# Kernel optimization log

Measured on AMD Instinct MI355X. Metric: run time of the kernel, lower is better.

The kernel has to match this reference:

```python
import jax, jax.numpy as jnp
import numpy as np


def setup_inputs() -> dict:
    key = jax.random.key(0)
    k1, k2, k3 = jax.random.split(key, 3)
    B, C_in, H, W = 16, 256, 64, 64
    C_out, KH, KW = 256, 3, 3
    x = jax.random.normal(k1, (B, C_in, H, W), dtype=jnp.float32)
    # kaiming-uniform-like scale for realism
    fan_in = C_in * KH * KW
    bound = 1.0 / np.sqrt(fan_in)
    weights = jax.random.normal(k2, (C_out, C_in, KH, KW), dtype=jnp.float32) * bound
    bias = jax.random.uniform(k3, (C_out,), dtype=jnp.float32, minval=-bound, maxval=bound)
    return {"x": x, "weights": weights, "bias": bias}


def reference(x, weights, bias):
    # Conv2dApproximation with approximation_enable=False is an exact conv2d:
    # input is unfolded to [B, C*kh*kw, oh, ow], weights to [C_out, C*kh*kw],
    # and the MultiApp kernel performs the exact MAC (see exact matmul backward).
    # stride=(1,1), padding=(0,0), dilation=(1,1) per init_kwargs.
    out = jax.lax.conv_general_dilated(
        x, weights,
        window_strides=(1, 1),
        padding=((0, 0), (0, 0)),
        rhs_dilation=(1, 1),
        dimension_numbers=("NCHW", "OIHW", "NCHW"),
    )
    return out + bias[None, :, None, None]
```

## Files before the change

kernel.cpp:

```cpp
#include <hip/hip_runtime.h>
#include <stdint.h>

typedef short short8 __attribute__((ext_vector_type(8)));
typedef float f32x4 __attribute__((ext_vector_type(4)));

#define AS1 __attribute__((address_space(1)))
#define AS3 __attribute__((address_space(3)))

__device__ __forceinline__ void gl_lds16(const void* g, void* l) {
  __builtin_amdgcn_global_load_lds((const AS1 unsigned int*)g,
                                   (AS3 unsigned int*)l, 16, 0, 0);
}

__device__ __forceinline__ unsigned short f2bf(float f) {
  union { float f; unsigned int u; } v; v.f = f;
  return (unsigned short)((v.u + (((v.u >> 16) & 1u) + 0x7fffu)) >> 16);
}

__global__ __launch_bounds__(256) void xpose_kernel(const float* __restrict__ x,
                                                    unsigned short* __restrict__ xt) {
  __shared__ float tile[64][68];
  const int bid = blockIdx.x;
  const int cchunk = bid & 3;
  const int y = (bid >> 2) & 63;
  const int b = bid >> 8;
  const int t = threadIdx.x;
  const int ci0 = cchunk * 64;

  const int cc = t >> 2;
  const int xo = (t & 3) * 16;
  const float* src = x + (((size_t)(b * 256 + ci0 + cc) * 64 + y) * 64 + xo);
  float4 v0 = ((const float4*)src)[0];
  float4 v1 = ((const float4*)src)[1];
  float4 v2 = ((const float4*)src)[2];
  float4 v3 = ((const float4*)src)[3];
  *(float4*)&tile[cc][xo + 0]  = v0;
  *(float4*)&tile[cc][xo + 4]  = v1;
  *(float4*)&tile[cc][xo + 8]  = v2;
  *(float4*)&tile[cc][xo + 12] = v3;
  __syncthreads();

  const int xpos = t >> 2;
  const int ccg = (t & 3) * 16;
  unsigned int pk[8];
#pragma unroll
  for (int e = 0; e < 8; ++e) {
    unsigned int lo = f2bf(tile[ccg + 2 * e][xpos]);
    unsigned int hi = f2bf(tile[ccg + 2 * e + 1][xpos]);
    pk[e] = lo | (hi << 16);
  }
  unsigned short* dst = xt + ((size_t)(b * 4096 + y * 64 + xpos) * 256 + ci0 + ccg);
  uint4 w0; w0.x = pk[0]; w0.y = pk[1]; w0.z = pk[2]; w0.w = pk[3];
  uint4 w1; w1.x = pk[4]; w1.y = pk[5]; w1.z = pk[6]; w1.w = pk[7];
  ((uint4*)dst)[0] = w0;
  ((uint4*)dst)[1] = w1;
}

__global__ __launch_bounds__(256) void wpack_kernel(const float* __restrict__ w,
                                                    unsigned short* __restrict__ wrp) {
  const int idx = blockIdx.x * 256 + threadIdx.x;
  const int ci = idx & 255;
  const int co = (idx >> 8) & 255;
  const int p = idx >> 16;
  wrp[idx] = f2bf(w[(size_t)(co * 256 + ci) * 9 + p]);
}

__global__ __launch_bounds__(512, 2) void conv_pipe(
    const unsigned short* __restrict__ xt,
    const unsigned short* __restrict__ wrp,
    const float* __restrict__ bias,
    float* __restrict__ out) {
  __shared__ unsigned short lds[2][32768];

  const int tid = threadIdx.x;
  const int lane = tid & 63;
  const int wv = tid >> 6;
  const int wm = wv >> 2;
  const int wn = wv & 3;
  const int bid = blockIdx.x;
  const int tile = (bid & 7) * 32 + (bid >> 3);
  const int b = tile >> 4;
  const int oh0 = (tile & 15) * 4;

  const int crow = tid >> 3;
  const int cslot = tid & 7;
  const int sw = cslot ^ (crow & 7);
  const unsigned short* gAbase = wrp + (size_t)crow * 256 + sw * 8;
  const unsigned short* gBbase[4];
#pragma unroll
  for (int cb = 0; cb < 4; ++cb) {
    const int y = min(oh0 + cb, 61);
    const int x = min(crow, 61);
    gBbase[cb] = xt + ((size_t)(b * 64 + y) * 64 + x) * 256 + sw * 8;
  }
  const unsigned dst_rc = crow * 64 + cslot * 8;

  const int l15 = lane & 15;
  int s8v[2];
  s8v[0] = (((lane >> 4)) ^ (lane & 7)) * 8;
  s8v[1] = (((lane >> 4) + 4) ^ (lane & 7)) * 8;
  int arow[8], brow[4];
#pragma unroll
  for (int a = 0; a < 8; ++a)
    arow[a] = (wm * 128 + (a >> 2) * 64 + (a & 3) * 16 + l15) * 64;
#pragma unroll
  for (int n = 0; n < 4; ++n)
    brow[n] = 16384 + (wn * 64 + n * 16 + l15) * 64;

  auto stageA = [&](int kt2, unsigned short* bufp) {
    const int tap = kt2 >> 2, ci0 = (kt2 & 3) * 64;
    const unsigned short* g = gAbase + tap * 65536 + ci0;
#pragma unroll
    for (int c = 0; c < 4; ++c)
      gl_lds16(g + c * 16384, bufp + c * 4096 + dst_rc);
  };
  auto stageB = [&](int kt2, unsigned short* bufp) {
    const int tap = kt2 >> 2, ci0 = (kt2 & 3) * 64;
    const int kh = (tap * 11) >> 5, kw = tap - kh * 3;
    const int off = (kh * 64 + kw) * 256 + ci0;
#pragma unroll
    for (int cb = 0; cb < 4; ++cb)
      gl_lds16(gBbase[cb] + off, bufp + (4 + cb) * 4096 + dst_rc);
  };

  f32x4 acc[8][4] = {};
  unsigned short* buf0 = &lds[0][0];
  unsigned short* buf1 = &lds[1][0];

  stageA(0, buf0);
  stageB(0, buf0);
  asm volatile("s_waitcnt vmcnt(0)" ::: "memory");
  __builtin_amdgcn_s_barrier();

  short8 a_cur[4], b_cur[4], a_nxt[4], b_nxt[4];
#pragma unroll
  for (int q = 0; q < 4; ++q) a_cur[q] = *(const short8*)(buf0 + arow[q] + s8v[0]);
#pragma unroll
  for (int n = 0; n < 4; ++n) b_cur[n] = *(const short8*)(buf0 + brow[n] + s8v[0]);

  for (int kt = 0; kt < 36; ++kt) {
    const unsigned short* buf = (kt & 1) ? buf1 : buf0;
    unsigned short* nbuf = (kt & 1) ? buf0 : buf1;

#pragma unroll
    for (int q = 0; q < 4; ++q) a_nxt[q] = *(const short8*)(buf + arow[4 + q] + s8v[0]);
    if (kt < 35) stageA(kt + 1, nbuf);
    __builtin_amdgcn_sched_barrier(0);
    __builtin_amdgcn_s_setprio(1);
#pragma unroll
    for (int q = 0; q < 4; ++q)
#pragma unroll
      for (int n = 0; n < 4; ++n)
        acc[q][n] = __builtin_amdgcn_mfma_f32_16x16x32_bf16(a_cur[q], b_cur[n], acc[q][n], 0, 0, 0);
    __builtin_amdgcn_s_setprio(0);

#pragma unroll
    for (int q = 0; q < 4; ++q) a_cur[q] = *(const short8*)(buf + arow[q] + s8v[1]);
#pragma unroll
    for (int n = 0; n < 4; ++n) b_nxt[n] = *(const short8*)(buf + brow[n] + s8v[1]);
    if (kt < 35) stageB(kt + 1, nbuf);
    __builtin_amdgcn_sched_barrier(0);
    __builtin_amdgcn_s_setprio(1);
#pragma unroll
    for (int q = 0; q < 4; ++q)
#pragma unroll
      for (int n = 0; n < 4; ++n)
        acc[4 + q][n] = __builtin_amdgcn_mfma_f32_16x16x32_bf16(a_nxt[q], b_cur[n], acc[4 + q][n], 0, 0, 0);
    __builtin_amdgcn_s_setprio(0);

#pragma unroll
    for (int q = 0; q < 4; ++q) a_nxt[q] = *(const short8*)(buf + arow[4 + q] + s8v[1]);
    __builtin_amdgcn_sched_barrier(0);
    __builtin_amdgcn_s_setprio(1);
#pragma unroll
    for (int q = 0; q < 4; ++q)
#pragma unroll
      for (int n = 0; n < 4; ++n)
        acc[q][n] = __builtin_amdgcn_mfma_f32_16x16x32_bf16(a_cur[q], b_nxt[n], acc[q][n], 0, 0, 0);
    __builtin_amdgcn_s_setprio(0);

    if (kt < 35) {
      asm volatile("s_waitcnt vmcnt(0)" ::: "memory");
      asm volatile("s_waitcnt lgkmcnt(0)" ::: "memory");
      __builtin_amdgcn_s_barrier();
#pragma unroll
      for (int q = 0; q < 4; ++q) a_cur[q] = *(const short8*)(nbuf + arow[q] + s8v[0]);
#pragma unroll
      for (int n = 0; n < 4; ++n) b_cur[n] = *(const short8*)(nbuf + brow[n] + s8v[0]);
    }
    __builtin_amdgcn_sched_barrier(0);
    __builtin_amdgcn_s_setprio(1);
#pragma unroll
    for (int q = 0; q < 4; ++q)
#pragma unroll
      for (int n = 0; n < 4; ++n)
        acc[4 + q][n] = __builtin_amdgcn_mfma_f32_16x16x32_bf16(a_nxt[q], b_nxt[n], acc[4 + q][n], 0, 0, 0);
    __builtin_amdgcn_s_setprio(0);
  }

  const int rb = (lane >> 4) * 4;
  const int colp = lane & 15;
#pragma unroll
  for (int a = 0; a < 8; ++a) {
    const int co = wm * 128 + (a >> 2) * 64 + (a & 3) * 16 + rb;
    float bv[4];
#pragma unroll
    for (int j = 0; j < 4; ++j) bv[j] = bias[co + j];
#pragma unroll
    for (int n = 0; n < 4; ++n) {
      const int px = wn * 64 + n * 16 + colp;
      const int prow = px >> 6, ow = px & 63;
      const int oh = oh0 + prow;
      if (ow < 62 && oh < 62) {
#pragma unroll
        for (int j = 0; j < 4; ++j)
          out[((size_t)(b * 256 + co + j) * 62 + oh) * 62 + ow] = acc[a][n][j] + bv[j];
      }
    }
  }
}

__global__ __launch_bounds__(256) void conv_naive(const float* __restrict__ x,
                                                  const float* __restrict__ wgt,
                                                  const float* __restrict__ bias,
                                                  float* __restrict__ out) {
  const size_t idx = (size_t)blockIdx.x * 256 + threadIdx.x;
  if (idx >= (size_t)16 * 256 * 62 * 62) return;
  const int ow = (int)(idx % 62);
  size_t r = idx / 62;
  const int oh = (int)(r % 62); r /= 62;
  const int co = (int)(r % 256);
  const int b = (int)(r / 256);
  float s = bias[co];
  for (int ci = 0; ci < 256; ++ci) {
    const float* xp = x + ((size_t)(b * 256 + ci) * 64 + oh) * 64 + ow;
    const float* wp = wgt + (size_t)(co * 256 + ci) * 9;
#pragma unroll
    for (int kh = 0; kh < 3; ++kh)
#pragma unroll
      for (int kw = 0; kw < 3; ++kw)
        s += xp[kh * 64 + kw] * wp[kh * 3 + kw];
  }
  out[idx] = s;
}

extern "C" void kernel_launch(void* const* d_in, const int* in_sizes, int n_in,
                              void* d_out, int out_size, void* d_ws, size_t ws_size,
                              hipStream_t stream) {
  const float* x = (const float*)d_in[0];
  const float* wgt = (const float*)d_in[1];
  const float* bias = (const float*)d_in[2];
  float* out = (float*)d_out;

  const size_t xt_elems = (size_t)16 * 64 * 64 * 256;
  const size_t wr_elems = (size_t)9 * 256 * 256;
  const size_t need = (xt_elems + wr_elems) * sizeof(unsigned short);

  if (ws_size < need) {
    conv_naive<<<61504, 256, 0, stream>>>(x, wgt, bias, out);
    return;
  }

  unsigned short* xt = (unsigned short*)d_ws;
  unsigned short* wrp = xt + xt_elems;

  xpose_kernel<<<4096, 256, 0, stream>>>(x, xt);
  wpack_kernel<<<2304, 256, 0, stream>>>(wgt, wrp);
  conv_pipe<<<256, 512, 0, stream>>>(xt, wrp, bias, out);
}
```

Measured before the change: 89.07 us.

## Shrink conv tiles to 128x128 with 256-thread blocks for more workgroups

Replaces the 256x256-tile, 512-thread conv kernel (256 workgroups) with a 128(co)x128(pixel) tile kernel using 256 threads, launched as 992 workgroups that split output channels into halves and cover two output rows each. This removes the wasted padded rows (62 of 64 rows are computed, not 64) and gives better occupancy and load balance across CUs. The cost is lower arithmetic intensity per tile, so more global/LDS traffic per MFMA, and A/B staging is merged into one point in the loop.

```diff
diff --git a/kernel.cpp b/kernel.cpp
--- a/kernel.cpp
+++ b/kernel.cpp
@@ -65,33 +65,37 @@
   wrp[idx] = f2bf(w[(size_t)(co * 256 + ci) * 9 + p]);
 }
 
-__global__ __launch_bounds__(512, 2) void conv_pipe(
+__global__ __launch_bounds__(256, 2) void conv_2blk(
     const unsigned short* __restrict__ xt,
     const unsigned short* __restrict__ wrp,
     const float* __restrict__ bias,
     float* __restrict__ out) {
-  __shared__ unsigned short lds[2][32768];
+  __shared__ unsigned short lds[2][16384];
 
   const int tid = threadIdx.x;
   const int lane = tid & 63;
   const int wv = tid >> 6;
-  const int wm = wv >> 2;
-  const int wn = wv & 3;
-  const int bid = blockIdx.x;
-  const int tile = (bid & 7) * 32 + (bid >> 3);
-  const int b = tile >> 4;
-  const int oh0 = (tile & 15) * 4;
+  const int wm = wv >> 1;
+  const int wn = wv & 1;
+  const int raw = blockIdx.x;
+  const int wg = (raw & 7) * 124 + (raw >> 3);
+  const int cohalf = (wg >= 496) ? 1 : 0;
+  const int pt = wg - cohalf * 496;
+  const int b = pt / 31;
+  const int oh0 = (pt - b * 31) * 2;
+  const int co0 = cohalf * 128;
 
   const int crow = tid >> 3;
   const int cslot = tid & 7;
   const int sw = cslot ^ (crow & 7);
-  const unsigned short* gAbase = wrp + (size_t)crow * 256 + sw * 8;
-  const unsigned short* gBbase[4];
+  const unsigned short* gA = wrp + (size_t)(co0 + crow) * 256 + sw * 8;
+  const unsigned short* gB[4];
 #pragma unroll
   for (int cb = 0; cb < 4; ++cb) {
-    const int y = min(oh0 + cb, 61);
-    const int x = min(crow, 61);
-    gBbase[cb] = xt + ((size_t)(b * 64 + y) * 64 + x) * 256 + sw * 8;
+    const int px = cb * 32 + crow;
+    const int y = min(oh0 + (px >> 6), 61);
+    const int xc = min(px & 63, 61);
+    gB[cb] = xt + ((size_t)(b * 64 + y) * 64 + xc) * 256 + sw * 8;
   }
   const unsigned dst_rc = crow * 64 + cslot * 8;
 
@@ -99,20 +103,20 @@
   int s8v[2];
   s8v[0] = (((lane >> 4)) ^ (lane & 7)) * 8;
   s8v[1] = (((lane >> 4) + 4) ^ (lane & 7)) * 8;
-  int arow[8], brow[4];
-#pragma unroll
-  for (int a = 0; a < 8; ++a)
-    arow[a] = (wm * 128 + (a >> 2) * 64 + (a & 3) * 16 + l15) * 64;
+  int arow[4], brow[4];
+#pragma unroll
+  for (int m = 0; m < 4; ++m)
+    arow[m] = (wm * 64 + m * 16 + l15) * 64;
 #pragma unroll
   for (int n = 0; n < 4; ++n)
-    brow[n] = 16384 + (wn * 64 + n * 16 + l15) * 64;
+    brow[n] = 8192 + (wn * 64 + n * 16 + l15) * 64;
 
   auto stageA = [&](int kt2, unsigned short* bufp) {
     const int tap = kt2 >> 2, ci0 = (kt2 & 3) * 64;
-    const unsigned short* g = gAbase + tap * 65536 + ci0;
+    const unsigned short* g = gA + tap * 65536 + ci0;
 #pragma unroll
     for (int c = 0; c < 4; ++c)
-      gl_lds16(g + c * 16384, bufp + c * 4096 + dst_rc);
+      gl_lds16(g + c * 8192, bufp + c * 2048 + dst_rc);
   };
   auto stageB = [&](int kt2, unsigned short* bufp) {
     const int tap = kt2 >> 2, ci0 = (kt2 & 3) * 64;
@@ -120,10 +124,10 @@
     const int off = (kh * 64 + kw) * 256 + ci0;
 #pragma unroll
     for (int cb = 0; cb < 4; ++cb)
-      gl_lds16(gBbase[cb] + off, bufp + (4 + cb) * 4096 + dst_rc);
+      gl_lds16(gB[cb] + off, bufp + 8192 + cb * 2048 + dst_rc);
   };
 
-  f32x4 acc[8][4] = {};
+  f32x4 acc[4][4] = {};
   unsigned short* buf0 = &lds[0][0];
   unsigned short* buf1 = &lds[1][0];
 
@@ -143,8 +147,10 @@
     unsigned short* nbuf = (kt & 1) ? buf0 : buf1;
 
 #pragma unroll
-    for (int q = 0; q < 4; ++q) a_nxt[q] = *(const short8*)(buf + arow[4 + q] + s8v[0]);
-    if (kt < 35) stageA(kt + 1, nbuf);
+    for (int q = 0; q < 4; ++q) a_nxt[q] = *(const short8*)(buf + arow[q] + s8v[1]);
+#pragma unroll
+    for (int n = 0; n < 4; ++n) b_nxt[n] = *(const short8*)(buf + brow[n] + s8v[1]);
+    if (kt < 35) { stageA(kt + 1, nbuf); stageB(kt + 1, nbuf); }
     __builtin_amdgcn_sched_barrier(0);
     __builtin_amdgcn_s_setprio(1);
 #pragma unroll
@@ -154,29 +160,13 @@
         acc[q][n] = __builtin_amdgcn_mfma_f32_16x16x32_bf16(a_cur[q], b_cur[n], acc[q][n], 0, 0, 0);
     __builtin_amdgcn_s_setprio(0);
 
-#pragma unroll
-    for (int q = 0; q < 4; ++q) a_cur[q] = *(const short8*)(buf + arow[q] + s8v[1]);
-#pragma unroll
-    for (int n = 0; n < 4; ++n) b_nxt[n] = *(const short8*)(buf + brow[n] + s8v[1]);
-    if (kt < 35) stageB(kt + 1, nbuf);
     __builtin_amdgcn_sched_barrier(0);
     __builtin_amdgcn_s_setprio(1);
 #pragma unroll
     for (int q = 0; q < 4; ++q)
 #pragma unroll
-      for (int n = 0; n < 4; ++n)
-        acc[4 + q][n] = __builtin_amdgcn_mfma_f32_16x16x32_bf16(a_nxt[q], b_cur[n], acc[4 + q][n], 0, 0, 0);
-    __builtin_amdgcn_s_setprio(0);
-
-#pragma unroll
-    for (int q = 0; q < 4; ++q) a_nxt[q] = *(const short8*)(buf + arow[4 + q] + s8v[1]);
-    __builtin_amdgcn_sched_barrier(0);
-    __builtin_amdgcn_s_setprio(1);
-#pragma unroll
-    for (int q = 0; q < 4; ++q)
-#pragma unroll
-      for (int n = 0; n < 4; ++n)
-        acc[q][n] = __builtin_amdgcn_mfma_f32_16x16x32_bf16(a_cur[q], b_nxt[n], acc[q][n], 0, 0, 0);
+      for (int n = 0; n < 2; ++n)
+        acc[q][n] = __builtin_amdgcn_mfma_f32_16x16x32_bf16(a_nxt[q], b_nxt[n], acc[q][n], 0, 0, 0);
     __builtin_amdgcn_s_setprio(0);
 
     if (kt < 35) {
@@ -188,21 +178,22 @@
 #pragma unroll
       for (int n = 0; n < 4; ++n) b_cur[n] = *(const short8*)(nbuf + brow[n] + s8v[0]);
     }
+
     __builtin_amdgcn_sched_barrier(0);
     __builtin_amdgcn_s_setprio(1);
 #pragma unroll
     for (int q = 0; q < 4; ++q)
 #pragma unroll
-      for (int n = 0; n < 4; ++n)
-        acc[4 + q][n] = __builtin_amdgcn_mfma_f32_16x16x32_bf16(a_nxt[q], b_nxt[n], acc[4 + q][n], 0, 0, 0);
+      for (int n = 2; n < 4; ++n)
+        acc[q][n] = __builtin_amdgcn_mfma_f32_16x16x32_bf16(a_nxt[q], b_nxt[n], acc[q][n], 0, 0, 0);
     __builtin_amdgcn_s_setprio(0);
   }
 
   const int rb = (lane >> 4) * 4;
   const int colp = lane & 15;
 #pragma unroll
-  for (int a = 0; a < 8; ++a) {
-    const int co = wm * 128 + (a >> 2) * 64 + (a & 3) * 16 + rb;
+  for (int m = 0; m < 4; ++m) {
+    const int co = co0 + wm * 64 + m * 16 + rb;
     float bv[4];
 #pragma unroll
     for (int j = 0; j < 4; ++j) bv[j] = bias[co + j];
@@ -211,10 +202,10 @@
       const int px = wn * 64 + n * 16 + colp;
       const int prow = px >> 6, ow = px & 63;
       const int oh = oh0 + prow;
-      if (ow < 62 && oh < 62) {
+      if (ow < 62) {
 #pragma unroll
         for (int j = 0; j < 4; ++j)
-          out[((size_t)(b * 256 + co + j) * 62 + oh) * 62 + ow] = acc[a][n][j] + bv[j];
+          out[((size_t)(b * 256 + co + j) * 62 + oh) * 62 + ow] = acc[m][n][j] + bv[j];
       }
     }
   }
@@ -266,5 +257,5 @@
 
   xpose_kernel<<<4096, 256, 0, stream>>>(x, xt);
   wpack_kernel<<<2304, 256, 0, stream>>>(wgt, wrp);
-  conv_pipe<<<256, 512, 0, stream>>>(xt, wrp, bias, out);
-}
+  conv_2blk<<<992, 256, 0, stream>>>(xt, wrp, bias, out);
+}
```

New measurement: 104.3 us. 1.17x slower.
